# Optimization experiments

Hardware: AMD Instinct MI355X
Metric: run time of the kernel (lower is better)

Reference implementation:

```python
import jax, jax.numpy as jnp
import numpy as np

DIM = 1024
N_HEADS = 16
HEAD_DIM = DIM // N_HEADS
B, T = 2, 2048


def setup_inputs() -> dict:
    key = jax.random.key(0)
    ks = jax.random.split(key, 5)
    x = jax.random.normal(ks[0], (B, T, DIM), dtype=jnp.float32)
    s = DIM ** -0.5
    Wq = jax.random.normal(ks[1], (DIM, DIM), dtype=jnp.float32) * s
    Wk = jax.random.normal(ks[2], (DIM, DIM), dtype=jnp.float32) * s
    Wv = jax.random.normal(ks[3], (DIM, DIM), dtype=jnp.float32) * s
    Wo = jax.random.normal(ks[4], (DIM, DIM), dtype=jnp.float32) * s
    # causal mask: 1 where attendable, 0 where masked (masked_fill on mask==0)
    mask = jnp.tril(jnp.ones((T, T), dtype=jnp.int32))[None, None, :, :]
    return {"x": x, "Wq": Wq, "Wk": Wk, "Wv": Wv, "Wo": Wo, "mask": mask}


def _rope_tables(seq_len, dim, dtype):
    inv_freq = 1.0 / (10000.0 ** (jnp.arange(0, dim, 2, dtype=jnp.float32) / dim))
    t = jnp.arange(seq_len, dtype=jnp.float32)
    freqs = jnp.outer(t, inv_freq)               # [T, dim/2]
    emb = jnp.concatenate([freqs, freqs], -1)    # [T, dim]
    return jnp.cos(emb).astype(dtype), jnp.sin(emb).astype(dtype)


def _rotate_half(t):
    h = t.shape[-1] // 2
    return jnp.concatenate([-t[..., h:], t[..., :h]], axis=-1)


def reference(x, Wq, Wk, Wv, Wo, mask):
    Bq, Tq, C = x.shape
    H, Dh = N_HEADS, C // N_HEADS
    q = (x @ Wq.T).reshape(Bq, Tq, H, Dh)
    k = (x @ Wk.T).reshape(Bq, Tq, H, Dh)
    v = (x @ Wv.T).reshape(Bq, Tq, H, Dh)
    cos, sin = _rope_tables(Tq, Dh, x.dtype)
    cos = cos[None, :, None, :]   # [1,T,1,Dh]
    sin = sin[None, :, None, :]
    q = q * cos + _rotate_half(q) * sin
    k = k * cos + _rotate_half(k) * sin
    scale = Dh ** -0.5
    # [B,H,T,T]
    attn = jnp.einsum('bqhd,bkhd->bhqk', q, k) * scale
    attn = jnp.where(mask == 0, jnp.float32(-jnp.inf).astype(attn.dtype), attn)
    attn = jax.nn.softmax(attn, axis=-1)
    out = jnp.einsum('bhqk,bkhd->bqhd', attn, v).reshape(Bq, Tq, C)
    return out @ Wo.T
```

## Files before the change

kernel.cpp:

```cpp
#include <hip/hip_runtime.h>
#include <stdint.h>


typedef float  f32x4  __attribute__((ext_vector_type(4)));
typedef float  f32x16 __attribute__((ext_vector_type(16)));
typedef __bf16 bf16x8 __attribute__((ext_vector_type(8)));
typedef unsigned int u32x2 __attribute__((ext_vector_type(2)));

#define GLDS16(gp, lp)                                                         \
  __builtin_amdgcn_global_load_lds(                                            \
      (const __attribute__((address_space(1))) void*)(gp),                     \
      (__attribute__((address_space(3))) void*)(lp), 16, 0, 0)

static __device__ __forceinline__ f32x4 zero4() {
  f32x4 z = {0.f, 0.f, 0.f, 0.f};
  return z;
}

static __device__ __forceinline__ bf16x8 cvt8(const float* __restrict__ p) {
  f32x4 u = *(const f32x4*)p;
  f32x4 v = *(const f32x4*)(p + 4);
  bf16x8 o;
#pragma unroll
  for (int j = 0; j < 4; ++j) o[j] = (__bf16)u[j];
#pragma unroll
  for (int j = 0; j < 4; ++j) o[4 + j] = (__bf16)v[j];
  return o;
}

__global__ __launch_bounds__(256) void prep(
    const float* __restrict__ x,
    const float* __restrict__ Wq, const float* __restrict__ Wk,
    const float* __restrict__ Wv, const float* __restrict__ Wo,
    __bf16* __restrict__ xb, __bf16* __restrict__ Wb)
{
  size_t g = ((size_t)blockIdx.x * 256 + threadIdx.x) * 8;
  if (g < (size_t)4194304) {
    *(bf16x8*)&xb[g] = cvt8(x + g);
  } else {
    size_t j = g - 4194304;
    int w = (int)(j >> 20);
    size_t off = j & 1048575;
    const float* src = (w == 0) ? Wq : (w == 1) ? Wk : (w == 2) ? Wv : Wo;
    *(bf16x8*)&Wb[(size_t)w * 1048576 + off] = cvt8(src + off);
  }
}

__global__ __launch_bounds__(256) void gemm_qkv(
    const __bf16* __restrict__ xb, const __bf16* __restrict__ Wb,
    __bf16* __restrict__ Qp, __bf16* __restrict__ Kp, __bf16* __restrict__ Vt)
{
  __shared__ __bf16 As[128 * 32];
  __shared__ __bf16 Bs[128 * 32];
  __shared__ __bf16 Es[4 * 16 * 72];

  const int tid  = threadIdx.x;
  const int lane = tid & 63;
  const int wid  = tid >> 6;
  const int quad = lane >> 4;
  const int l16  = lane & 15;
  const int wm   = (wid >> 1) * 64;
  const int wn   = (wid & 1) * 64;

  const int lin = blockIdx.x;
  const int n0  = (lin & 7) * 128;
  const int r2  = lin >> 3;
  const int z   = r2 % 3;
  const int m0  = (r2 / 3) * 128;
  const __bf16* Bt = Wb + (size_t)z * 1048576;

  const int r0 = tid >> 2, c0 = tid & 3;
  const int r1 = (tid + 256) >> 2;

  f32x4 acc[4][4];
  for (int i = 0; i < 4; ++i)
    for (int j = 0; j < 4; ++j) acc[i][j] = zero4();

  for (int k0 = 0; k0 < 1024; k0 += 32) {
    __syncthreads();
    GLDS16(xb + (size_t)(m0 + r0) * 1024 + k0 + c0 * 8, &As[(size_t)tid * 8]);
    GLDS16(xb + (size_t)(m0 + r1) * 1024 + k0 + c0 * 8, &As[(size_t)(tid + 256) * 8]);
    GLDS16(Bt + (size_t)(n0 + r0) * 1024 + k0 + c0 * 8, &Bs[(size_t)tid * 8]);
    GLDS16(Bt + (size_t)(n0 + r1) * 1024 + k0 + c0 * 8, &Bs[(size_t)(tid + 256) * 8]);
    __syncthreads();

    bf16x8 af[4], bfr[4];
    for (int i = 0; i < 4; ++i)
      af[i] = *(const bf16x8*)&As[(wm + i * 16 + l16) * 32 + quad * 8];
    for (int i = 0; i < 4; ++i)
      bfr[i] = *(const bf16x8*)&Bs[(wn + i * 16 + l16) * 32 + quad * 8];
    for (int mt = 0; mt < 4; ++mt)
      for (int nt = 0; nt < 4; ++nt)
        acc[mt][nt] = __builtin_amdgcn_mfma_f32_16x16x32_bf16(
            af[mt], bfr[nt], acc[mt][nt], 0, 0, 0);
  }

  const int h = (n0 + wn) >> 6;
  __bf16* es = &Es[wid * 1152];
  const int rl = lane >> 3, ch = lane & 7;

  if (z < 2) {
    const float c0f = -13.287712379549449f / 32.0f;
    const float f0 = exp2f((float)l16 * c0f);
    const float f1 = exp2f((float)(16 + l16) * c0f);
    const float SC = (z == 0) ? 0.125f * 1.44269504088896340736f : 1.0f;
    for (int mt = 0; mt < 4; ++mt)
      for (int r = 0; r < 4; ++r) {
        int gm = m0 + wm + mt * 16 + 4 * quad + r;
        float t = (float)(gm & 2047);
        for (int nt = 0; nt < 2; ++nt) {
          float ang = t * (nt ? f1 : f0);
          float cv = __cosf(ang) * SC, sv = __sinf(ang) * SC;
          float lo = acc[mt][nt][r], hi = acc[mt][nt + 2][r];
          acc[mt][nt][r]     = lo * cv - hi * sv;
          acc[mt][nt + 2][r] = hi * cv + lo * sv;
        }
      }
    __bf16* dst = (z == 0) ? Qp : Kp;
    for (int mt = 0; mt < 4; ++mt) {
      for (int nt = 0; nt < 4; ++nt)
        for (int r = 0; r < 4; ++r)
          es[(4 * quad + r) * 72 + nt * 16 + l16] = (__bf16)acc[mt][nt][r];
      size_t g0 = (size_t)(m0 + wm + mt * 16 + rl) * 1024 + n0 + wn + ch * 8;
      *(bf16x8*)&dst[g0]            = *(const bf16x8*)&es[rl * 72 + ch * 8];
      *(bf16x8*)&dst[g0 + 8 * 1024] = *(const bf16x8*)&es[(rl + 8) * 72 + ch * 8];
    }
  } else {
    const int b = m0 >> 11;
    const size_t hb = (size_t)(b * 16 + h) * 64;
    const int tt = (m0 + wm) & 2047;
    for (int nt = 0; nt < 4; ++nt) {
      for (int mt = 0; mt < 4; ++mt)
        for (int r = 0; r < 4; ++r)
          es[l16 * 72 + mt * 16 + 4 * quad + r] = (__bf16)acc[mt][nt][r];
      size_t g0 = (hb + nt * 16 + rl) * 2048 + tt + ch * 8;
      *(bf16x8*)&Vt[g0]                     = *(const bf16x8*)&es[rl * 72 + ch * 8];
      *(bf16x8*)&Vt[g0 + (size_t)8 * 2048]  = *(const bf16x8*)&es[(rl + 8) * 72 + ch * 8];
    }
  }
}

__global__ __launch_bounds__(256) void attn_fwd(
    __bf16* QA, const __bf16* __restrict__ Kp,
    const __bf16* __restrict__ Vt)
{
  __shared__ __bf16 Ks[2][64 * 64];
  __shared__ __bf16 Vs[2][64 * 64];

  const int tid  = threadIdx.x;
  const int lane = tid & 63, wid = tid >> 6;
  const int hl = lane >> 5, lq = lane & 31, lq7 = lq & 7;
  const int qh = wid & 1, kh = wid >> 1;

  const int L  = blockIdx.x;
  const int j  = L >> 3;
  const int qb = 31 - (j >> 2);
  const int bh = (L & 7) * 4 + (j & 3);
  const int b = bh >> 4, h = bh & 15;
  const int q0 = qb * 64;

  const size_t rowb = (size_t)b * 2048;
  const __bf16* Vb = Vt + (size_t)bh * 64 * 2048;

  const int srow = lane >> 3;
  const int scol = ((lane & 7) ^ srow) * 8;
  const int ck0 = wid * 2, ck1 = wid * 2 + 1;

  const int iql = qh * 32 + lq;

  bf16x8 qa[4];
#pragma unroll
  for (int ks = 0; ks < 4; ++ks)
    qa[ks] = *(const bf16x8*)
        &QA[(rowb + q0 + iql) * 1024 + h * 64 + ks * 16 + hl * 8];

  f32x16 oacc[2];
#pragma unroll
  for (int dt = 0; dt < 2; ++dt)
#pragma unroll
    for (int r = 0; r < 16; ++r) oacc[dt][r] = 0.f;
  float l_i = 0.f;

  const int kcmax = qb;

  GLDS16(Kp + (rowb + ck0 * 8 + srow) * 1024 + h * 64 + scol, &Ks[0][ck0 * 512]);
  GLDS16(Kp + (rowb + ck1 * 8 + srow) * 1024 + h * 64 + scol, &Ks[0][ck1 * 512]);
  GLDS16(Vb + (size_t)(ck0 * 8 + srow) * 2048 + scol, &Vs[0][ck0 * 512]);
  GLDS16(Vb + (size_t)(ck1 * 8 + srow) * 2048 + scol, &Vs[0][ck1 * 512]);
  __syncthreads();

  for (int kc = 0; kc <= kcmax; ++kc) {
    const int c = kc & 1;
    if (kc < kcmax) {
      const int t0 = (kc + 1) * 64;
      GLDS16(Kp + (rowb + t0 + ck0 * 8 + srow) * 1024 + h * 64 + scol,
             &Ks[c ^ 1][ck0 * 512]);
      GLDS16(Kp + (rowb + t0 + ck1 * 8 + srow) * 1024 + h * 64 + scol,
             &Ks[c ^ 1][ck1 * 512]);
      GLDS16(Vb + (size_t)(ck0 * 8 + srow) * 2048 + t0 + scol,
             &Vs[c ^ 1][ck0 * 512]);
      GLDS16(Vb + (size_t)(ck1 * 8 + srow) * 2048 + t0 + scol,
             &Vs[c ^ 1][ck1 * 512]);
    }

    const __bf16* Ksb = Ks[c];
    const __bf16* Vsb = Vs[c];

    f32x16 sacc;
#pragma unroll
    for (int r = 0; r < 16; ++r) sacc[r] = -16.f;
    __builtin_amdgcn_s_setprio(1);
#pragma unroll
    for (int ks = 0; ks < 4; ++ks) {
      bf16x8 kf = *(const bf16x8*)
          &Ksb[(kh * 32 + lq) * 64 + (((2 * ks + hl) ^ lq7) * 8)];
      sacc = __builtin_amdgcn_mfma_f32_32x32x16_bf16(kf, qa[ks], sacc, 0, 0, 0);
    }
    __builtin_amdgcn_s_setprio(0);

    const bool diag = (kc == kcmax);
    float p[16];
    float rsum = 0.f;
#pragma unroll
    for (int r = 0; r < 16; ++r) {
      float s = sacc[r];
      if (diag) {
        int kp = kh * 32 + (r & 3) + 8 * (r >> 2) + 4 * hl;
        if (kp > iql) s = -1e30f;
      }
      p[r] = __builtin_amdgcn_exp2f(s);
      rsum += p[r];
    }
    rsum += __shfl_xor(rsum, 32, 64);
    l_i += rsum;

    unsigned int cpk[8];
#pragma unroll
    for (int i = 0; i < 8; ++i)
      asm("v_cvt_pk_bf16_f32 %0, %1, %2"
          : "=v"(cpk[i]) : "v"(p[2 * i]), "v"(p[2 * i + 1]));
    bf16x8 pb[2];
#pragma unroll
    for (int k2 = 0; k2 < 2; ++k2) {
      unsigned int a0 = cpk[4 * k2 + 0], b0 = cpk[4 * k2 + 2];
      unsigned int a1 = cpk[4 * k2 + 1], b1 = cpk[4 * k2 + 3];
      asm("v_permlane32_swap_b32 %0, %1" : "+v"(a0), "+v"(b0));
      asm("v_permlane32_swap_b32 %0, %1" : "+v"(a1), "+v"(b1));
      union { unsigned int w[4]; bf16x8 v; } u;
      u.w[0] = a0; u.w[1] = a1; u.w[2] = b0; u.w[3] = b1;
      pb[k2] = u.v;
    }

    __builtin_amdgcn_s_setprio(1);
#pragma unroll
    for (int dt = 0; dt < 2; ++dt)
#pragma unroll
      for (int k2 = 0; k2 < 2; ++k2) {
        bf16x8 vf = *(const bf16x8*)
            &Vsb[(dt * 32 + lq) * 64 + (((4 * kh + 2 * k2 + hl) ^ lq7) * 8)];
        oacc[dt] = __builtin_amdgcn_mfma_f32_32x32x16_bf16(
            vf, pb[k2], oacc[dt], 0, 0, 0);
      }
    __builtin_amdgcn_s_setprio(0);

    __syncthreads();
  }

  float* Osf = (float*)&Ks[0][0];
  float* Lsf = (float*)&Vs[0][0];
  if (kh == 1) {
#pragma unroll
    for (int dt = 0; dt < 2; ++dt) {
      float* base = &Osf[((qh * 2 + dt) * 64 + lane) * 16];
#pragma unroll
      for (int g = 0; g < 4; ++g) {
        f32x4 w = {oacc[dt][4 * g], oacc[dt][4 * g + 1],
                   oacc[dt][4 * g + 2], oacc[dt][4 * g + 3]};
        *(f32x4*)&base[4 * g] = w;
      }
    }
    Lsf[qh * 64 + lane] = l_i;
  }
  __syncthreads();
  if (kh == 0) {
#pragma unroll
    for (int dt = 0; dt < 2; ++dt) {
      const float* base = &Osf[((qh * 2 + dt) * 64 + lane) * 16];
#pragma unroll
      for (int g = 0; g < 4; ++g) {
        f32x4 w = *(const f32x4*)&base[4 * g];
#pragma unroll
        for (int e = 0; e < 4; ++e) oacc[dt][4 * g + e] += w[e];
      }
    }
    float inv = 1.0f / (l_i + Lsf[qh * 64 + lane]);
#pragma unroll
    for (int dt = 0; dt < 2; ++dt)
#pragma unroll
      for (int g = 0; g < 4; ++g) {
        float a = oacc[dt][4 * g]     * inv, bb = oacc[dt][4 * g + 1] * inv;
        float cc = oacc[dt][4 * g + 2] * inv, dd = oacc[dt][4 * g + 3] * inv;
        unsigned int w0, w1;
        asm("v_cvt_pk_bf16_f32 %0, %1, %2" : "=v"(w0) : "v"(a), "v"(bb));
        asm("v_cvt_pk_bf16_f32 %0, %1, %2" : "=v"(w1) : "v"(cc), "v"(dd));
        u32x2 wv = {w0, w1};
        *(u32x2*)&QA[(rowb + q0 + iql) * 1024 + h * 64 + dt * 32 + 8 * g + 4 * hl] = wv;
      }
  }
}

__global__ __launch_bounds__(256) void gemm_out(
    const __bf16* __restrict__ AO, const __bf16* __restrict__ Wob,
    float* __restrict__ Of)
{
  __shared__ __bf16 As[128 * 32];
  __shared__ __bf16 Bs[128 * 32];
  __shared__ float  EsF[4 * 16 * 68];

  const int tid  = threadIdx.x;
  const int lane = tid & 63;
  const int wid  = tid >> 6;
  const int quad = lane >> 4;
  const int l16  = lane & 15;
  const int wm   = (wid >> 1) * 64;
  const int wn   = (wid & 1) * 64;
  const int lin = blockIdx.x;
  const int n0  = (lin & 7) * 128;
  const int m0  = (lin >> 3) * 128;

  const int r0 = tid >> 2, c0 = tid & 3;
  const int r1 = (tid + 256) >> 2;

  f32x4 acc[4][4];
  for (int i = 0; i < 4; ++i)
    for (int j = 0; j < 4; ++j) acc[i][j] = zero4();

  for (int k0 = 0; k0 < 1024; k0 += 32) {
    __syncthreads();
    GLDS16(AO  + (size_t)(m0 + r0) * 1024 + k0 + c0 * 8, &As[(size_t)tid * 8]);
    GLDS16(AO  + (size_t)(m0 + r1) * 1024 + k0 + c0 * 8, &As[(size_t)(tid + 256) * 8]);
    GLDS16(Wob + (size_t)(n0 + r0) * 1024 + k0 + c0 * 8, &Bs[(size_t)tid * 8]);
    GLDS16(Wob + (size_t)(n0 + r1) * 1024 + k0 + c0 * 8, &Bs[(size_t)(tid + 256) * 8]);
    __syncthreads();

    bf16x8 af[4], bfr[4];
    for (int i = 0; i < 4; ++i)
      af[i] = *(const bf16x8*)&As[(wm + i * 16 + l16) * 32 + quad * 8];
    for (int i = 0; i < 4; ++i)
      bfr[i] = *(const bf16x8*)&Bs[(wn + i * 16 + l16) * 32 + quad * 8];
    for (int mt = 0; mt < 4; ++mt)
      for (int nt = 0; nt < 4; ++nt)
        acc[mt][nt] = __builtin_amdgcn_mfma_f32_16x16x32_bf16(
            af[mt], bfr[nt], acc[mt][nt], 0, 0, 0);
  }

  float* es = &EsF[wid * 1088];
  const int rl = lane >> 4, ch = lane & 15;
  for (int mt = 0; mt < 4; ++mt) {
    for (int nt = 0; nt < 4; ++nt)
      for (int r = 0; r < 4; ++r)
        es[(4 * quad + r) * 68 + nt * 16 + l16] = acc[mt][nt][r];
    size_t g0 = (size_t)(m0 + wm + mt * 16 + rl) * 1024 + n0 + wn + ch * 4;
    *(f32x4*)&Of[g0]             = *(const f32x4*)&es[rl * 68 + ch * 4];
    *(f32x4*)&Of[g0 + 4 * 1024]  = *(const f32x4*)&es[(rl + 4) * 68 + ch * 4];
    *(f32x4*)&Of[g0 + 8 * 1024]  = *(const f32x4*)&es[(rl + 8) * 68 + ch * 4];
    *(f32x4*)&Of[g0 + 12 * 1024] = *(const f32x4*)&es[(rl + 12) * 68 + ch * 4];
  }
}

__global__ __launch_bounds__(256) void copy_bf16x8(
    const __bf16* __restrict__ src, __bf16* __restrict__ dst)
{
  size_t i = ((size_t)blockIdx.x * 256 + threadIdx.x) * 8;
  *(bf16x8*)&dst[i] = *(const bf16x8*)&src[i];
}

extern "C" void kernel_launch(void* const* d_in, const int* in_sizes, int n_in,
                              void* d_out, int out_size, void* d_ws, size_t ws_size,
                              hipStream_t stream) {
  const float* x  = (const float*)d_in[0];
  const float* Wq = (const float*)d_in[1];
  const float* Wk = (const float*)d_in[2];
  const float* Wv = (const float*)d_in[3];
  const float* Wo = (const float*)d_in[4];
  float* out = (float*)d_out;

  const size_t NELT = (size_t)4194304;
  __bf16* Qp = (__bf16*)d_ws;
  __bf16* Kp = Qp + NELT;
  __bf16* Vt = Kp + NELT;
  __bf16* xb = (__bf16*)d_out;
  __bf16* Wb = xb + NELT;

  prep<<<dim3(4096), 256, 0, stream>>>(x, Wq, Wk, Wv, Wo, xb, Wb);
  gemm_qkv<<<dim3(768), 256, 0, stream>>>(xb, Wb, Qp, Kp, Vt);
  attn_fwd<<<dim3(1024), 256, 0, stream>>>(Qp, Kp, Vt);
  copy_bf16x8<<<dim3(512), 256, 0, stream>>>(Wb + 3 * NELT / 4, Kp);
  gemm_out<<<dim3(256), 256, 0, stream>>>(Qp, Kp, out);
}
```

Measured before the change: 193.9 us.

## Double K-tile depth, XOR-swizzle LDS, and remap block order in projection GEMMs

Both the QKV and output-projection GEMMs now stage 64-wide K slices per iteration instead of 32, which halves the number of barrier pairs and global-to-LDS rounds. The LDS layout uses an XOR swizzle on the 16-byte chunk index so that fragment reads from the 64-element rows avoid bank conflicts. The block index is also remapped so that consecutive blocks walk the N tiles of the same M rows, which is meant to improve L2 reuse of the activation tiles. In exchange LDS use per block doubles, which may reduce occupancy, and the pipeline is still not double-buffered.

```diff
diff --git a/kernel.cpp b/kernel.cpp
--- a/kernel.cpp
+++ b/kernel.cpp
@@ -50,8 +50,8 @@
     const __bf16* __restrict__ xb, const __bf16* __restrict__ Wb,
     __bf16* __restrict__ Qp, __bf16* __restrict__ Kp, __bf16* __restrict__ Vt)
 {
-  __shared__ __bf16 As[128 * 32];
-  __shared__ __bf16 Bs[128 * 32];
+  __shared__ __bf16 As[128 * 64];
+  __shared__ __bf16 Bs[128 * 64];
   __shared__ __bf16 Es[4 * 16 * 72];
 
   const int tid  = threadIdx.x;
@@ -62,37 +62,51 @@
   const int wm   = (wid >> 1) * 64;
   const int wn   = (wid & 1) * 64;
 
-  const int lin = blockIdx.x;
-  const int n0  = (lin & 7) * 128;
-  const int r2  = lin >> 3;
-  const int z   = r2 % 3;
-  const int m0  = (r2 / 3) * 128;
+  const int L  = blockIdx.x;
+  const int t  = L >> 3;
+  const int n0 = (t & 7) * 128;
+  const int zm = (L & 7) * 12 + (t >> 3);
+  const int z  = zm % 3;
+  const int m0 = (zm / 3) * 128;
   const __bf16* Bt = Wb + (size_t)z * 1048576;
 
-  const int r0 = tid >> 2, c0 = tid & 3;
-  const int r1 = (tid + 256) >> 2;
+  const int sr  = tid >> 3;
+  const int scx = ((tid & 7) ^ (sr & 7)) * 8;
+  const int fx  = l16 & 7;
 
   f32x4 acc[4][4];
   for (int i = 0; i < 4; ++i)
     for (int j = 0; j < 4; ++j) acc[i][j] = zero4();
 
-  for (int k0 = 0; k0 < 1024; k0 += 32) {
+  for (int k0 = 0; k0 < 1024; k0 += 64) {
     __syncthreads();
-    GLDS16(xb + (size_t)(m0 + r0) * 1024 + k0 + c0 * 8, &As[(size_t)tid * 8]);
-    GLDS16(xb + (size_t)(m0 + r1) * 1024 + k0 + c0 * 8, &As[(size_t)(tid + 256) * 8]);
-    GLDS16(Bt + (size_t)(n0 + r0) * 1024 + k0 + c0 * 8, &Bs[(size_t)tid * 8]);
-    GLDS16(Bt + (size_t)(n0 + r1) * 1024 + k0 + c0 * 8, &Bs[(size_t)(tid + 256) * 8]);
+#pragma unroll
+    for (int c = 0; c < 4; ++c) {
+      GLDS16(xb + (size_t)(m0 + c * 32 + sr) * 1024 + k0 + scx,
+             &As[c * 2048 + (size_t)tid * 8]);
+      GLDS16(Bt + (size_t)(n0 + c * 32 + sr) * 1024 + k0 + scx,
+             &Bs[c * 2048 + (size_t)tid * 8]);
+    }
     __syncthreads();
 
-    bf16x8 af[4], bfr[4];
-    for (int i = 0; i < 4; ++i)
-      af[i] = *(const bf16x8*)&As[(wm + i * 16 + l16) * 32 + quad * 8];
-    for (int i = 0; i < 4; ++i)
-      bfr[i] = *(const bf16x8*)&Bs[(wn + i * 16 + l16) * 32 + quad * 8];
-    for (int mt = 0; mt < 4; ++mt)
-      for (int nt = 0; nt < 4; ++nt)
-        acc[mt][nt] = __builtin_amdgcn_mfma_f32_16x16x32_bf16(
-            af[mt], bfr[nt], acc[mt][nt], 0, 0, 0);
+#pragma unroll
+    for (int ks = 0; ks < 2; ++ks) {
+      bf16x8 af[4], bfr[4];
+#pragma unroll
+      for (int i = 0; i < 4; ++i)
+        af[i] = *(const bf16x8*)
+            &As[(wm + i * 16 + l16) * 64 + ((ks * 4 + quad) ^ fx) * 8];
+#pragma unroll
+      for (int i = 0; i < 4; ++i)
+        bfr[i] = *(const bf16x8*)
+            &Bs[(wn + i * 16 + l16) * 64 + ((ks * 4 + quad) ^ fx) * 8];
+#pragma unroll
+      for (int mt = 0; mt < 4; ++mt)
+#pragma unroll
+        for (int nt = 0; nt < 4; ++nt)
+          acc[mt][nt] = __builtin_amdgcn_mfma_f32_16x16x32_bf16(
+              af[mt], bfr[nt], acc[mt][nt], 0, 0, 0);
+    }
   }
 
   const int h = (n0 + wn) >> 6;
@@ -107,9 +121,9 @@
     for (int mt = 0; mt < 4; ++mt)
       for (int r = 0; r < 4; ++r) {
         int gm = m0 + wm + mt * 16 + 4 * quad + r;
-        float t = (float)(gm & 2047);
+        float tt = (float)(gm & 2047);
         for (int nt = 0; nt < 2; ++nt) {
-          float ang = t * (nt ? f1 : f0);
+          float ang = tt * (nt ? f1 : f0);
           float cv = __cosf(ang) * SC, sv = __sinf(ang) * SC;
           float lo = acc[mt][nt][r], hi = acc[mt][nt + 2][r];
           acc[mt][nt][r]     = lo * cv - hi * sv;
@@ -313,8 +327,8 @@
     const __bf16* __restrict__ AO, const __bf16* __restrict__ Wob,
     float* __restrict__ Of)
 {
-  __shared__ __bf16 As[128 * 32];
-  __shared__ __bf16 Bs[128 * 32];
+  __shared__ __bf16 As[128 * 64];
+  __shared__ __bf16 Bs[128 * 64];
   __shared__ float  EsF[4 * 16 * 68];
 
   const int tid  = threadIdx.x;
@@ -324,34 +338,49 @@
   const int l16  = lane & 15;
   const int wm   = (wid >> 1) * 64;
   const int wn   = (wid & 1) * 64;
-  const int lin = blockIdx.x;
-  const int n0  = (lin & 7) * 128;
-  const int m0  = (lin >> 3) * 128;
-
-  const int r0 = tid >> 2, c0 = tid & 3;
-  const int r1 = (tid + 256) >> 2;
+
+  const int L  = blockIdx.x;
+  const int t  = L >> 3;
+  const int n0 = (t & 7) * 128;
+  const int m0 = ((L & 7) * 4 + (t >> 3)) * 128;
+
+  const int sr  = tid >> 3;
+  const int scx = ((tid & 7) ^ (sr & 7)) * 8;
+  const int fx  = l16 & 7;
 
   f32x4 acc[4][4];
   for (int i = 0; i < 4; ++i)
     for (int j = 0; j < 4; ++j) acc[i][j] = zero4();
 
-  for (int k0 = 0; k0 < 1024; k0 += 32) {
+  for (int k0 = 0; k0 < 1024; k0 += 64) {
     __syncthreads();
-    GLDS16(AO  + (size_t)(m0 + r0) * 1024 + k0 + c0 * 8, &As[(size_t)tid * 8]);
-    GLDS16(AO  + (size_t)(m0 + r1) * 1024 + k0 + c0 * 8, &As[(size_t)(tid + 256) * 8]);
-    GLDS16(Wob + (size_t)(n0 + r0) * 1024 + k0 + c0 * 8, &Bs[(size_t)tid * 8]);
-    GLDS16(Wob + (size_t)(n0 + r1) * 1024 + k0 + c0 * 8, &Bs[(size_t)(tid + 256) * 8]);
+#pragma unroll
+    for (int c = 0; c < 4; ++c) {
+      GLDS16(AO  + (size_t)(m0 + c * 32 + sr) * 1024 + k0 + scx,
+             &As[c * 2048 + (size_t)tid * 8]);
+      GLDS16(Wob + (size_t)(n0 + c * 32 + sr) * 1024 + k0 + scx,
+             &Bs[c * 2048 + (size_t)tid * 8]);
+    }
     __syncthreads();
 
-    bf16x8 af[4], bfr[4];
-    for (int i = 0; i < 4; ++i)
-      af[i] = *(const bf16x8*)&As[(wm + i * 16 + l16) * 32 + quad * 8];
-    for (int i = 0; i < 4; ++i)
-      bfr[i] = *(const bf16x8*)&Bs[(wn + i * 16 + l16) * 32 + quad * 8];
-    for (int mt = 0; mt < 4; ++mt)
-      for (int nt = 0; nt < 4; ++nt)
-        acc[mt][nt] = __builtin_amdgcn_mfma_f32_16x16x32_bf16(
-            af[mt], bfr[nt], acc[mt][nt], 0, 0, 0);
+#pragma unroll
+    for (int ks = 0; ks < 2; ++ks) {
+      bf16x8 af[4], bfr[4];
+#pragma unroll
+      for (int i = 0; i < 4; ++i)
+        af[i] = *(const bf16x8*)
+            &As[(wm + i * 16 + l16) * 64 + ((ks * 4 + quad) ^ fx) * 8];
+#pragma unroll
+      for (int i = 0; i < 4; ++i)
+        bfr[i] = *(const bf16x8*)
+            &Bs[(wn + i * 16 + l16) * 64 + ((ks * 4 + quad) ^ fx) * 8];
+#pragma unroll
+      for (int mt = 0; mt < 4; ++mt)
+#pragma unroll
+        for (int nt = 0; nt < 4; ++nt)
+          acc[mt][nt] = __builtin_amdgcn_mfma_f32_16x16x32_bf16(
+              af[mt], bfr[nt], acc[mt][nt], 0, 0, 0);
+    }
   }
 
   float* es = &EsF[wid * 1088];
```

Result: no change. 197.0 us (+1.6%).
